# Kernel tuning notes

Hardware: AMD Instinct MI355X
Metric: run time of the kernel (lower is better)

The kernel has to match this reference:

```python
import jax, jax.numpy as jnp
import numpy as np

B, T, C = 4, 2048, 1024
H = 16
D = C // H  # head_dim = 64


def setup_inputs() -> dict:
    key = jax.random.key(0)
    k1, k2, k3, k4, k5 = jax.random.split(key, 5)
    s = 0.02
    return {
        "x": jax.random.normal(k1, (B, T, C), dtype=jnp.float32),
        "W_qkv": jax.random.normal(k2, (C, 3 * C), dtype=jnp.float32) * s,
        "b_qkv": jax.random.normal(k3, (3 * C,), dtype=jnp.float32) * s,
        "W_o": jax.random.normal(k4, (C, C), dtype=jnp.float32) * s,
        "b_o": jax.random.normal(k5, (C,), dtype=jnp.float32) * s,
    }


def reference(x, W_qkv, b_qkv, W_o, b_o):
    b, t, c = x.shape
    scaling = D ** (-0.5)
    qkv = x @ W_qkv + b_qkv                      # [B,T,3C]
    q, k, v = jnp.split(qkv, 3, axis=-1)         # each [B,T,C]
    q = q.reshape(b, t, H, D).transpose(0, 2, 1, 3)  # [B,H,T,D]
    k = k.reshape(b, t, H, D).transpose(0, 2, 1, 3)
    v = v.reshape(b, t, H, D).transpose(0, 2, 1, 3)
    scores = jnp.einsum("bhqd,bhkd->bhqk", q, k) * scaling  # [B,H,T,T]
    mask = jnp.tril(jnp.ones((t, t), dtype=bool))            # causal
    scores = jnp.where(mask[None, None, :, :], scores, -jnp.inf)
    probs = jax.nn.softmax(scores, axis=-1)
    out = jnp.einsum("bhqk,bhkd->bhqd", probs, v)            # [B,H,T,D]
    out = out.transpose(0, 2, 1, 3).reshape(b, t, c)         # [B,T,C]
    return out @ W_o + b_o
```

## Files before the change

kernel.cpp:

```cpp
#include <hip/hip_runtime.h>
#include <hip/hip_bf16.h>

typedef unsigned short ushort_t;
typedef __attribute__((ext_vector_type(8))) short short8;
typedef __attribute__((ext_vector_type(4))) float floatx4;
typedef __attribute__((ext_vector_type(2))) unsigned uint2v;
typedef __attribute__((ext_vector_type(4))) unsigned uint4v;

#define B_ 4
#define T_ 2048
#define C_ 1024
#define H_ 16
#define D_ 64
#define BT_ (B_ * T_)
#define N3C (3 * C_)

#define KSC 0.18033688011112042f

__device__ __forceinline__ ushort_t f2bf(float f) {
    unsigned u = __float_as_uint(f);
    u += 0x7FFF + ((u >> 16) & 1);
    return (ushort_t)(u >> 16);
}
__device__ __forceinline__ unsigned pack2bf(float a, float b) {
    __hip_bfloat162 h = __float22bfloat162_rn(make_float2(a, b));
    return *(unsigned*)&h;
}

__device__ __forceinline__ void gload16(const ushort_t* g, ushort_t* l) {
    __builtin_amdgcn_global_load_lds((const __attribute__((address_space(1))) void*)g,
                                     (__attribute__((address_space(3))) void*)l, 16, 0, 0);
}

__global__ void prep_k(const float* __restrict__ x, ushort_t* __restrict__ xb,
                       const float* __restrict__ Wqkv, ushort_t* __restrict__ WqkvT,
                       const float* __restrict__ Wo, ushort_t* __restrict__ WoT) {
    __shared__ ushort_t t[32][33];
    int id = blockIdx.x;
    if (id < 4096) {
        size_t i = ((size_t)id * 256 + threadIdx.x) * 8;
        const float* xf = x + i;
        float4 a = *(const float4*)xf;
        float4 b = *(const float4*)(xf + 4);
        short8 o;
        o[0] = (short)f2bf(a.x); o[1] = (short)f2bf(a.y);
        o[2] = (short)f2bf(a.z); o[3] = (short)f2bf(a.w);
        o[4] = (short)f2bf(b.x); o[5] = (short)f2bf(b.y);
        o[6] = (short)f2bf(b.z); o[7] = (short)f2bf(b.w);
        *(short8*)&xb[i] = o;
        return;
    }
    int tt = id - 4096;
    int bx = tt & 127, by = tt >> 7;
    const float* in;
    ushort_t* out;
    int Nc, bc;
    if (bx < 96) { in = Wqkv; out = WqkvT; Nc = N3C; bc = bx * 32; }
    else         { in = Wo;   out = WoT;   Nc = C_;  bc = (bx - 96) * 32; }
    int br = by * 32;
    int lx = threadIdx.x & 31, ly = threadIdx.x >> 5;
#pragma unroll
    for (int i = 0; i < 4; ++i) {
        int r = ly + i * 8;
        t[r][lx] = f2bf(in[(size_t)(br + r) * Nc + bc + lx]);
    }
    __syncthreads();
#pragma unroll
    for (int i = 0; i < 4; ++i) {
        int r = ly + i * 8;
        out[(size_t)(bc + r) * C_ + br + lx] = t[lx][r];
    }
}

__global__ void vtrans_k(const ushort_t* __restrict__ in, ushort_t* __restrict__ out) {
    __shared__ ushort_t t[32][33];
    int bh = blockIdx.z;
    const ushort_t* I = in + (size_t)bh * T_ * D_;
    ushort_t* O = out + (size_t)bh * D_ * T_;
    int bt = blockIdx.x * 32, bd = blockIdx.y * 32;
    int lx = threadIdx.x & 31, ly = threadIdx.x >> 5;
#pragma unroll
    for (int i = 0; i < 4; ++i) {
        int r = ly + i * 8;
        t[r][lx] = I[(size_t)(bt + r) * D_ + bd + lx];
    }
    __syncthreads();
#pragma unroll
    for (int i = 0; i < 4; ++i) {
        int r = ly + i * 8;
        O[(size_t)(bd + r) * T_ + bt + lx] = t[lx][r];
    }
}

template <int MODE>
__launch_bounds__(256)
__global__ void gemm_bt(const ushort_t* __restrict__ A, const ushort_t* __restrict__ Bt,
                        const float* __restrict__ bias, float* __restrict__ Cout,
                        ushort_t* __restrict__ Qo, ushort_t* __restrict__ Ko,
                        ushort_t* __restrict__ Vo, int M, int N, int K) {
    __shared__ __align__(16) ushort_t Alds[2][128 * 32];
    __shared__ __align__(16) ushort_t Blds[2][128 * 32];
    int tid = threadIdx.x;
    int wave = tid >> 6, lane = tid & 63;
    int bm = blockIdx.x * 128, bn = blockIdx.y * 128;
    int wr = (wave >> 1) * 64, wc = (wave & 1) * 64;
    int lm = lane & 15, lk = (lane >> 4) * 8, lq = lane >> 4;

    floatx4 acc[4][4] = {};

    int srow = tid >> 2;
    int scol = (tid & 3) * 8;
    const ushort_t* Ab = A + (size_t)(bm + srow) * K + scol;
    const ushort_t* Bb = Bt + (size_t)(bn + srow) * K + scol;
    int lo0 = wave * 512, lo1 = 2048 + wave * 512;
    size_t rowskip = (size_t)64 * K;

    gload16(Ab, &Alds[0][lo0]);
    gload16(Ab + rowskip, &Alds[0][lo1]);
    gload16(Bb, &Blds[0][lo0]);
    gload16(Bb + rowskip, &Blds[0][lo1]);
    __syncthreads();

    int cur = 0;
    for (int k0 = 0; k0 < K; k0 += 32) {
        if (k0 + 32 < K) {
            gload16(Ab + k0 + 32, &Alds[cur ^ 1][lo0]);
            gload16(Ab + k0 + 32 + rowskip, &Alds[cur ^ 1][lo1]);
            gload16(Bb + k0 + 32, &Blds[cur ^ 1][lo0]);
            gload16(Bb + k0 + 32 + rowskip, &Blds[cur ^ 1][lo1]);
        }
        short8 af[4], bf[4];
#pragma unroll
        for (int i = 0; i < 4; ++i)
            af[i] = *(const short8*)&Alds[cur][(wr + i * 16 + lm) * 32 + lk];
#pragma unroll
        for (int i = 0; i < 4; ++i)
            bf[i] = *(const short8*)&Blds[cur][(wc + i * 16 + lm) * 32 + lk];
#pragma unroll
        for (int mi = 0; mi < 4; ++mi)
#pragma unroll
            for (int ni = 0; ni < 4; ++ni)
                acc[mi][ni] = __builtin_amdgcn_mfma_f32_16x16x32_bf16(
                    af[mi], bf[ni], acc[mi][ni], 0, 0, 0);
        __syncthreads();
        cur ^= 1;
    }

#pragma unroll
    for (int mi = 0; mi < 4; ++mi) {
#pragma unroll
        for (int ni = 0; ni < 4; ++ni) {
            int col = bn + wc + ni * 16 + lm;
            float bv = bias[col];
#pragma unroll
            for (int r = 0; r < 4; ++r) {
                int row = bm + wr + mi * 16 + lq * 4 + r;
                float v = acc[mi][ni][r] + bv;
                if (MODE == 0) {
                    Cout[(size_t)row * N + col] = v;
                } else {
                    int b = row >> 11, t = row & (T_ - 1);
                    int which = col >> 10, c = col & (C_ - 1);
                    int h = c >> 6, d = c & 63;
                    int bh = b * H_ + h;
                    size_t idx = ((size_t)bh * T_ + t) * D_ + d;
                    if (which == 0)
                        Qo[idx] = f2bf(v * KSC);
                    else if (which == 1)
                        Ko[idx] = f2bf(v);
                    else
                        Vo[idx] = f2bf(v);
                }
            }
        }
    }
}

__launch_bounds__(512)
__global__ void attn_k(const ushort_t* __restrict__ Q, const ushort_t* __restrict__ K,
                       const ushort_t* __restrict__ Vt, ushort_t* __restrict__ O) {
    __shared__ __align__(16) ushort_t KV[2][2][64 * 64];

    int tid = threadIdx.x, wave = tid >> 6, lane = tid & 63;
    int id = blockIdx.x;
    int xcd = id & 7, j = id >> 3;
    int q = j & 7, g = j >> 3;
    int bh = xcd + 8 * g;
    int b = bh >> 4, h = bh & 15;
    int lm = lane & 15, lq = lane >> 4, m7 = lane & 7;

    const ushort_t* Qp = Q + (size_t)bh * T_ * D_;
    const ushort_t* Kp = K + (size_t)bh * T_ * D_;
    const ushort_t* Vp = Vt + (size_t)bh * D_ * T_;
    ushort_t* Ob = O + ((size_t)b * T_) * C_ + h * D_;

    int sr = tid >> 3;
    int sc = (tid & 7) ^ (sr & 7);
    const ushort_t* Kst = Kp + (size_t)sr * D_ + sc * 8;
    const ushort_t* Vst = Vp + (size_t)sr * T_ + sc * 8;
    int ldsb = wave * 512;

    short8 onesf = {};
    if (lm == 0) {
#pragma unroll
        for (int jj = 0; jj < 8; ++jj) onesf[jj] = (short)0x3F80;
    }

    int cur = 0;
#pragma unroll
    for (int pass = 0; pass < 2; ++pass) {
        int band = pass ? q : 15 - q;
        int m0 = band * 128 + wave * 16;
        int ntw = 2 * band + 2;

        short8 qf0 = *(const short8*)&Qp[(size_t)(m0 + lm) * D_ + lq * 8];
        short8 qf1 = *(const short8*)&Qp[(size_t)(m0 + lm) * D_ + 32 + lq * 8];

        floatx4 oacc[5] = {};

        gload16(Kst, &KV[cur][0][ldsb]);
        gload16(Vst, &KV[cur][1][ldsb]);
        __syncthreads();

        for (int it = 0; it < ntw; ++it) {
            if (it + 1 < ntw) {
                size_t kv0n = (size_t)(it + 1) * 64;
                gload16(Kst + kv0n * D_, &KV[cur ^ 1][0][ldsb]);
                gload16(Vst + kv0n, &KV[cur ^ 1][1][ldsb]);
            }
            int kv0 = it * 64;
            if (kv0 <= m0 + 15) {
                const ushort_t* Kb = &KV[cur][0][0];
                const ushort_t* Vb = &KV[cur][1][0];

                short8 kf[4][2], vf[4][2];
#pragma unroll
                for (int nt = 0; nt < 4; ++nt) {
                    kf[nt][0] = *(const short8*)&Kb[(nt * 16 + lm) * 64 + ((lq ^ m7) * 8)];
                    kf[nt][1] = *(const short8*)&Kb[(nt * 16 + lm) * 64 + (((lq + 4) ^ m7) * 8)];
                }

                floatx4 st[4] = {};
                __builtin_amdgcn_s_setprio(1);
#pragma unroll
                for (int nt = 0; nt < 4; ++nt) {
                    st[nt] = __builtin_amdgcn_mfma_f32_16x16x32_bf16(kf[nt][0], qf0, st[nt], 0, 0, 0);
                    st[nt] = __builtin_amdgcn_mfma_f32_16x16x32_bf16(kf[nt][1], qf1, st[nt], 0, 0, 0);
                }
                __builtin_amdgcn_s_setprio(0);

#pragma unroll
                for (int dt = 0; dt < 4; ++dt) {
                    vf[dt][0] = *(const short8*)&Vb[(dt * 16 + lm) * 64 + ((lq ^ m7) * 8)];
                    vf[dt][1] = *(const short8*)&Vb[(dt * 16 + lm) * 64 + (((lq + 4) ^ m7) * 8)];
                }

                if (kv0 + 63 > m0) {
                    int mg = m0 + lm;
#pragma unroll
                    for (int nt = 0; nt < 4; ++nt)
#pragma unroll
                        for (int r = 0; r < 4; ++r) {
                            int kvg = kv0 + nt * 16 + lq * 4 + r;
                            if (kvg > mg) st[nt][r] = -__builtin_inff();
                        }
                }

                unsigned e0 = pack2bf(__builtin_amdgcn_exp2f(st[0][0]), __builtin_amdgcn_exp2f(st[0][1]));
                unsigned e1 = pack2bf(__builtin_amdgcn_exp2f(st[0][2]), __builtin_amdgcn_exp2f(st[0][3]));
                unsigned e2 = pack2bf(__builtin_amdgcn_exp2f(st[1][0]), __builtin_amdgcn_exp2f(st[1][1]));
                unsigned e3 = pack2bf(__builtin_amdgcn_exp2f(st[1][2]), __builtin_amdgcn_exp2f(st[1][3]));
                unsigned e4 = pack2bf(__builtin_amdgcn_exp2f(st[2][0]), __builtin_amdgcn_exp2f(st[2][1]));
                unsigned e5 = pack2bf(__builtin_amdgcn_exp2f(st[2][2]), __builtin_amdgcn_exp2f(st[2][3]));
                unsigned e6 = pack2bf(__builtin_amdgcn_exp2f(st[3][0]), __builtin_amdgcn_exp2f(st[3][1]));
                unsigned e7 = pack2bf(__builtin_amdgcn_exp2f(st[3][2]), __builtin_amdgcn_exp2f(st[3][3]));

                uint2v ra = __builtin_amdgcn_permlane32_swap(e0, e2, false, false);
                uint2v wa = __builtin_amdgcn_permlane16_swap(ra[0], ra[1], false, false);
                uint2v rb = __builtin_amdgcn_permlane32_swap(e1, e3, false, false);
                uint2v wb = __builtin_amdgcn_permlane16_swap(rb[0], rb[1], false, false);
                uint2v rc = __builtin_amdgcn_permlane32_swap(e4, e6, false, false);
                uint2v wc = __builtin_amdgcn_permlane16_swap(rc[0], rc[1], false, false);
                uint2v rd = __builtin_amdgcn_permlane32_swap(e5, e7, false, false);
                uint2v wd = __builtin_amdgcn_permlane16_swap(rd[0], rd[1], false, false);

                short8 pb0 = __builtin_bit_cast(short8, (uint4v){wa[0], wb[0], wa[1], wb[1]});
                short8 pb1 = __builtin_bit_cast(short8, (uint4v){wc[0], wd[0], wc[1], wd[1]});

                __builtin_amdgcn_s_setprio(1);
#pragma unroll
                for (int dt = 0; dt < 4; ++dt) {
                    oacc[dt] = __builtin_amdgcn_mfma_f32_16x16x32_bf16(vf[dt][0], pb0, oacc[dt], 0, 0, 0);
                    oacc[dt] = __builtin_amdgcn_mfma_f32_16x16x32_bf16(vf[dt][1], pb1, oacc[dt], 0, 0, 0);
                }
                oacc[4] = __builtin_amdgcn_mfma_f32_16x16x32_bf16(onesf, pb0, oacc[4], 0, 0, 0);
                oacc[4] = __builtin_amdgcn_mfma_f32_16x16x32_bf16(onesf, pb1, oacc[4], 0, 0, 0);
                __builtin_amdgcn_s_setprio(0);
            }

            __syncthreads();
            cur ^= 1;
        }

        float li = __shfl(oacc[4][0], lm, 64);
        float inv = 1.0f / li;
        int tg = m0 + lm;
#pragma unroll
        for (int dt = 0; dt < 4; ++dt) {
            uint2 pk;
            pk.x = pack2bf(oacc[dt][0] * inv, oacc[dt][1] * inv);
            pk.y = pack2bf(oacc[dt][2] * inv, oacc[dt][3] * inv);
            *(uint2*)&Ob[(size_t)tg * C_ + dt * 16 + lq * 4] = pk;
        }
    }
}

extern "C" void kernel_launch(void* const* d_in, const int* in_sizes, int n_in,
                              void* d_out, int out_size, void* d_ws, size_t ws_size,
                              hipStream_t stream) {
    const float* x    = (const float*)d_in[0];
    const float* Wqkv = (const float*)d_in[1];
    const float* bqkv = (const float*)d_in[2];
    const float* Wo   = (const float*)d_in[3];
    const float* bo   = (const float*)d_in[4];

    ushort_t* ws = (ushort_t*)d_ws;
    ushort_t* WqkvT = ws;
    ushort_t* WoT   = WqkvT + (size_t)N3C * C_;
    ushort_t* Xb    = WoT + (size_t)C_ * C_;
    ushort_t* Qs    = Xb + (size_t)BT_ * C_;
    ushort_t* Ks    = Qs + (size_t)BT_ * C_;
    ushort_t* Vs    = Ks + (size_t)BT_ * C_;
    ushort_t* Attn  = Vs + (size_t)BT_ * C_;

    prep_k<<<8192, 256, 0, stream>>>(x, Xb, Wqkv, WqkvT, Wo, WoT);
    gemm_bt<1><<<dim3(BT_ / 128, N3C / 128), 256, 0, stream>>>(
        Xb, WqkvT, bqkv, nullptr, Qs, Ks, Attn, BT_, N3C, C_);
    vtrans_k<<<dim3(T_ / 32, D_ / 32, B_ * H_), 256, 0, stream>>>(Attn, Vs);
    attn_k<<<512, 512, 0, stream>>>(Qs, Ks, Vs, Attn);
    gemm_bt<0><<<dim3(BT_ / 128, C_ / 128), 256, 0, stream>>>(
        Attn, WoT, bo, (float*)d_out, nullptr, nullptr, nullptr, BT_, C_, C_);
}
```

Before: 244.4 us.

## Triple-buffer GEMM LDS tiles with two-stage-ahead async prefetch

The GEMM's LDS staging grows from two buffers to three, so global loads run two K-steps ahead instead of one. The per-iteration __syncthreads becomes a partial vmcnt wait that leaves the newest tile's loads in flight, followed by a raw s_barrier and a sched_barrier. The aim is to hide more global memory latency behind MFMA work. In exchange LDS use rises by half, which may lower occupancy, and correctness now relies on the hand-written vmcnt counts matching the four loads issued per step.

```diff
diff --git a/kernel.cpp b/kernel.cpp
--- a/kernel.cpp
+++ b/kernel.cpp
@@ -98,8 +98,8 @@
                         const float* __restrict__ bias, float* __restrict__ Cout,
                         ushort_t* __restrict__ Qo, ushort_t* __restrict__ Ko,
                         ushort_t* __restrict__ Vo, int M, int N, int K) {
-    __shared__ __align__(16) ushort_t Alds[2][128 * 32];
-    __shared__ __align__(16) ushort_t Blds[2][128 * 32];
+    __shared__ __align__(16) ushort_t Alds[3][128 * 32];
+    __shared__ __align__(16) ushort_t Blds[3][128 * 32];
     int tid = threadIdx.x;
     int wave = tid >> 6, lane = tid & 63;
     int bm = blockIdx.x * 128, bn = blockIdx.y * 128;
@@ -119,15 +119,27 @@
     gload16(Ab + rowskip, &Alds[0][lo1]);
     gload16(Bb, &Blds[0][lo0]);
     gload16(Bb + rowskip, &Blds[0][lo1]);
-    __syncthreads();
+    if (K > 32) {
+        gload16(Ab + 32, &Alds[1][lo0]);
+        gload16(Ab + 32 + rowskip, &Alds[1][lo1]);
+        gload16(Bb + 32, &Blds[1][lo0]);
+        gload16(Bb + 32 + rowskip, &Blds[1][lo1]);
+        asm volatile("s_waitcnt vmcnt(4)" ::: "memory");
+    } else {
+        asm volatile("s_waitcnt vmcnt(0)" ::: "memory");
+    }
+    __builtin_amdgcn_s_barrier();
+    __builtin_amdgcn_sched_barrier(0);
 
     int cur = 0;
     for (int k0 = 0; k0 < K; k0 += 32) {
-        if (k0 + 32 < K) {
-            gload16(Ab + k0 + 32, &Alds[cur ^ 1][lo0]);
-            gload16(Ab + k0 + 32 + rowskip, &Alds[cur ^ 1][lo1]);
-            gload16(Bb + k0 + 32, &Blds[cur ^ 1][lo0]);
-            gload16(Bb + k0 + 32 + rowskip, &Blds[cur ^ 1][lo1]);
+        int nxt = (cur == 2) ? 0 : cur + 1;
+        int nn = (nxt == 2) ? 0 : nxt + 1;
+        if (k0 + 64 < K) {
+            gload16(Ab + k0 + 64, &Alds[nn][lo0]);
+            gload16(Ab + k0 + 64 + rowskip, &Alds[nn][lo1]);
+            gload16(Bb + k0 + 64, &Blds[nn][lo0]);
+            gload16(Bb + k0 + 64 + rowskip, &Blds[nn][lo1]);
         }
         short8 af[4], bf[4];
 #pragma unroll
@@ -142,8 +154,14 @@
             for (int ni = 0; ni < 4; ++ni)
                 acc[mi][ni] = __builtin_amdgcn_mfma_f32_16x16x32_bf16(
                     af[mi], bf[ni], acc[mi][ni], 0, 0, 0);
-        __syncthreads();
-        cur ^= 1;
+        if (k0 + 64 < K) {
+            asm volatile("s_waitcnt vmcnt(4)" ::: "memory");
+        } else {
+            asm volatile("s_waitcnt vmcnt(0)" ::: "memory");
+        }
+        __builtin_amdgcn_s_barrier();
+        __builtin_amdgcn_sched_barrier(0);
+        cur = nxt;
     }
 
 #pragma unroll
```

Result: no change. 242.3 us (-0.9%).
